# Optimization experiments

Hardware: AMD Instinct MI355X
Metric: run time of the kernel (lower is better)

The kernel has to match this reference:

```python
import jax, jax.numpy as jnp
import numpy as np

B, N, E, D, N_NODE = 512, 64, 64, 256, 200000
NEG = -9e15
ALPHA = 0.2  # leaky-relu slope from HGNN_ATT(..., 0.2, ...)


def _hgat_layer(x, adj_mask, w2, w3, a, a2, wc, w=None):
    """HyperGraphAttentionLayerSparse (HyperGAT), dense-masked vectorized form.
    x: [B,N,d_in], adj_mask: [B,E,N] bool. Returns (node [B,N,d], edge [B,E,d]).
    Eval mode: dropout is identity. concat=False so no ELU on output."""
    d = w2.shape[1]
    x4 = x @ w2                                            # [B,N,d]
    if w is not None:                                      # transfer=True path
        x = x @ w
    # node->edge attention: score = leakyrelu([word_context; x4_node] @ a), independent of edge idx
    s1 = jax.nn.leaky_relu(jnp.dot(wc, a[:d, 0]) + x4 @ a[d:, 0], ALPHA)   # [B,N]
    att_edge = jax.nn.softmax(jnp.where(adj_mask, s1[:, None, :], NEG), axis=2)  # [B,E,N]
    edge = att_edge @ x                                    # [B,E,d]
    edge4 = edge @ w3                                      # [B,E,d]
    # edge->node attention: score = leakyrelu([x4_node; edge4_edge] @ a2)
    s_pair = jax.nn.leaky_relu((x4 @ a2[:d, 0])[:, None, :] + (edge4 @ a2[d:, 0])[:, :, None], ALPHA)  # [B,E,N]
    att_node = jax.nn.softmax(jnp.swapaxes(jnp.where(adj_mask, s_pair, NEG), 1, 2), axis=2)  # [B,N,E]
    node = att_node @ edge                                 # [B,N,d]
    return node, edge


def setup_inputs() -> dict:
    key = jax.random.key(0)
    ks = jax.random.split(key, 16)
    stdv = 1.0 / np.sqrt(D)  # SessionGraph.reset_parameters uniform(-stdv, stdv)
    u = lambda k, shape: jax.random.uniform(k, shape, jnp.float32, -stdv, stdv)
    return {
        "inputs": jax.random.randint(ks[0], (B, N), 0, N_NODE, dtype=jnp.int32),
        "HT": (jax.random.uniform(ks[1], (B, E, N)) < 0.3).astype(jnp.int32),
        "G": jnp.zeros((1,), jnp.float32),
        "EG": jnp.zeros((1,), jnp.float32),
        "emb_w": u(ks[2], (N_NODE, D)),
        "emb2_w": u(ks[3], (N_NODE, D)),
        "g1_w2": u(ks[4], (D, D)),
        "g1_w3": u(ks[5], (D, D)),
        "g1_a": u(ks[6], (2 * D, 1)),
        "g1_a2": u(ks[7], (2 * D, 1)),
        "g1_wc": u(ks[8], (D,)),
        "g2_w": u(ks[9], (D, D)),
        "g2_w2": u(ks[10], (D, D)),
        "g2_w3": u(ks[11], (D, D)),
        "g2_a": u(ks[12], (2 * D, 1)),
        "g2_a2": u(ks[13], (2 * D, 1)),
        "g2_wc": u(ks[14], (D,)),
    }


def reference(inputs, HT, G, EG, emb_w, emb2_w, g1_w2, g1_w3, g1_a, g1_a2, g1_wc,
              g2_w, g2_w2, g2_w3, g2_a, g2_a2, g2_wc):
    adj_mask = HT > 0
    x = emb_w[inputs]                                      # [B,N,D] embedding gather
    residual = x
    # HGNN_ATT with step=2: gat1 (transfer=False) + residual, gat2 (transfer=True) + residual
    x, _ = _hgat_layer(x, adj_mask, g1_w2, g1_w3, g1_a, g1_a2, g1_wc)
    x = x + residual
    x, _ = _hgat_layer(x, adj_mask, g2_w2, g2_w3, g2_a, g2_a2, g2_wc, g2_w)
    x = x + residual
    nodes2 = emb2_w[inputs]                                # second embedding gather
    return (x, x, nodes2)  # (nodes, hidden, nodes2); hidden aliases nodes in the original
```

## Files before the change

kernel.cpp:

```cpp
#include <hip/hip_runtime.h>

#define BB 512
#define NN 64
#define EE 64
#define DD 256
#define BND (BB * NN * DD)
#define SA 68

typedef __attribute__((ext_vector_type(8))) short s8v;
typedef __attribute__((ext_vector_type(4))) float f4v;
typedef __attribute__((ext_vector_type(8))) unsigned short u16x8;

__device__ __forceinline__ unsigned short f2bf(float f) {
    unsigned int x = __float_as_uint(f);
    x = x + 0x7fffu + ((x >> 16) & 1u);
    return (unsigned short)(x >> 16);
}
__device__ __forceinline__ float bf2f(unsigned short u) {
    return __uint_as_float(((unsigned int)u) << 16);
}
__device__ __forceinline__ float lrelu(float v) { return v > 0.f ? v : 0.2f * v; }

#define WS_PREP  0
#define WS_P3B   8192
#define WS_WFRAG 12288

__global__ void prep_dots(const float* __restrict__ w2a, const float* __restrict__ w3a,
                          const float* __restrict__ aa, const float* __restrict__ a2a,
                          const float* __restrict__ wca,
                          const float* __restrict__ w2b, const float* __restrict__ w3b,
                          const float* __restrict__ ab, const float* __restrict__ a2b,
                          const float* __restrict__ wcb,
                          float* __restrict__ prep, float* __restrict__ p3b_ws) {
    const int t = threadIdx.x;
    const int blk = blockIdx.x;
    const int layer = blk >> 3;
    const int r0 = (blk & 7) * 32;
    __shared__ float vhi[256], v2lo[256], v2hi[256], red[256];
    const float* w2 = layer ? w2b : w2a;
    const float* w3 = layer ? w3b : w3a;
    const float* av = layer ? ab : aa;
    const float* a2 = layer ? a2b : a2a;
    vhi[t] = av[256 + t];
    v2lo[t] = a2[t];
    v2hi[t] = a2[256 + t];
    __syncthreads();
    const int row = r0 + (t >> 3), q = t & 7;
    const float* w2r = w2 + (size_t)row * DD + q * 32;
    const float* w3r = w3 + (size_t)row * DD + q * 32;
    float s1 = 0.f, s2 = 0.f, s3 = 0.f;
    #pragma unroll
    for (int c = 0; c < 8; c++) {
        float4 v = *(const float4*)&w2r[c * 4];
        float4 u = *(const float4*)&w3r[c * 4];
        float4 p1 = *(const float4*)&vhi[q * 32 + c * 4];
        float4 p2 = *(const float4*)&v2lo[q * 32 + c * 4];
        float4 p3 = *(const float4*)&v2hi[q * 32 + c * 4];
        s1 = fmaf(v.x, p1.x, fmaf(v.y, p1.y, fmaf(v.z, p1.z, fmaf(v.w, p1.w, s1))));
        s2 = fmaf(v.x, p2.x, fmaf(v.y, p2.y, fmaf(v.z, p2.z, fmaf(v.w, p2.w, s2))));
        s3 = fmaf(u.x, p3.x, fmaf(u.y, p3.y, fmaf(u.z, p3.z, fmaf(u.w, p3.w, s3))));
    }
    s1 += __shfl_xor(s1, 1); s1 += __shfl_xor(s1, 2); s1 += __shfl_xor(s1, 4);
    s2 += __shfl_xor(s2, 1); s2 += __shfl_xor(s2, 2); s2 += __shfl_xor(s2, 4);
    s3 += __shfl_xor(s3, 1); s3 += __shfl_xor(s3, 2); s3 += __shfl_xor(s3, 4);
    if (q == 0) {
        if (layer == 0) { prep[row] = s1; prep[256 + row] = s2; prep[512 + row] = s3; }
        else { prep[1024 + row] = s1; prep[1280 + row] = s2; p3b_ws[row] = s3; }
    }
    if ((blk & 7) == 0) {
        red[t] = layer ? (wcb[t] * ab[t]) : (wca[t] * aa[t]);
        __syncthreads();
        for (int o = 128; o > 0; o >>= 1) { if (t < o) red[t] += red[t + o]; __syncthreads(); }
        if (t == 0) prep[layer ? 1792 : 768] = red[0];
    }
}

__global__ void prep2_pack(const float* __restrict__ wtr, const float* __restrict__ p3b_ws,
                           float* __restrict__ prep, unsigned short* __restrict__ wfrag) {
    const int t = threadIdx.x, blk = blockIdx.x;
    __shared__ float p3[256];
    if (blk < 8) {
        p3[t] = p3b_ws[t];
        __syncthreads();
        const int row = blk * 32 + (t >> 3), q = t & 7;
        const float* wr = wtr + (size_t)row * DD + q * 32;
        float s = 0.f;
        #pragma unroll
        for (int c = 0; c < 8; c++) {
            float4 v = *(const float4*)&wr[c * 4];
            float4 p = *(const float4*)&p3[q * 32 + c * 4];
            s = fmaf(v.x, p.x, fmaf(v.y, p.y, fmaf(v.z, p.z, fmaf(v.w, p.w, s))));
        }
        s += __shfl_xor(s, 1); s += __shfl_xor(s, 2); s += __shfl_xor(s, 4);
        if (q == 0) prep[1536 + row] = s;
    } else {
        int gid = (blk - 8) * 256 + t;
        int l = gid & 63, frag = gid >> 6;
        int kc = frag >> 4, nt = frag & 15;
        int kb = kc * 32 + (l >> 4) * 8;
        int n = nt * 16 + (l & 15);
        u16x8 u;
        #pragma unroll
        for (int j = 0; j < 8; j++) u[j] = f2bf(wtr[(size_t)(kb + j) * DD + n]);
        *(u16x8*)(wfrag + (size_t)gid * 8) = u;
    }
}

__launch_bounds__(512, 4)
__global__ void mega(const int* __restrict__ inputs, const int* __restrict__ HT,
                     const float* __restrict__ emb_w, const float* __restrict__ emb2_w,
                     const float* __restrict__ prep, const unsigned short* __restrict__ wfrag,
                     float* __restrict__ out) {
    __shared__ unsigned short bufA[256 * SA];
    __shared__ unsigned short RA[64 * SA];
    __shared__ unsigned short RB[64 * SA];
    __shared__ unsigned short RC[64 * SA];
    __shared__ unsigned short RD[64 * SA];
    __shared__ unsigned short pvs[6 * 256];
    __shared__ unsigned short Debf[64];
    __shared__ float dvs[384];
    __shared__ float db2[192];
    __shared__ float u1f[64], invdef[64], invdnf[64];
    __shared__ unsigned long long mE[64], mN[64];
    __shared__ int idxs[64];

    const int b = blockIdx.x;
    const int t = threadIdx.x;
    const int lane = t & 63;
    const int w8 = t >> 6;
    const int l15 = lane & 15, lh = lane >> 4;

    if (t < 64) idxs[t] = inputs[b * 64 + t];
    for (int i = t; i < 1536; i += 512) {
        int off = i + (((i >> 8) >= 3) ? 256 : 0);
        pvs[i] = f2bf(prep[off]);
    }
    {
        const int rw = t >> 3, q8 = t & 7;
        const int idx = inputs[b * 64 + rw];
        const float* src = emb_w + (size_t)idx * DD + q8 * 32;
        #pragma unroll
        for (int c = 0; c < 8; c++) {
            float4 v = ((const float4*)src)[c];
            ushort4 u;
            u.x = f2bf(v.x); u.y = f2bf(v.y); u.z = f2bf(v.z); u.w = f2bf(v.w);
            *(ushort4*)&bufA[rw * 264 + q8 * 32 + c * 4] = u;
        }
    }
    float4 n2r[8];
    #pragma unroll
    for (int c = 0; c < 8; c++) {
        int i = t + 512 * c;
        int n = i >> 6, cc = i & 63;
        int idx = inputs[b * 64 + n];
        n2r[c] = ((const float4*)(emb2_w + (size_t)idx * DD))[cc];
    }
    #pragma unroll
    for (int i = 0; i < 8; i++) {
        int e = w8 * 8 + i;
        int hx = HT[((size_t)b * EE + e) * NN + lane];
        unsigned long long m = __ballot(hx > 0);
        if (lane == 0) mE[e] = m;
    }
    __syncthreads();

    if (w8 < 4) {
        const int wtile = w8 * 16;
        const int j = (l15 < 6) ? l15 : 5;
        f4v acc = {0.f, 0.f, 0.f, 0.f};
        #pragma unroll
        for (int kc = 0; kc < 8; kc++) {
            s8v a = *(const s8v*)&bufA[(wtile + l15) * 264 + kc * 32 + lh * 8];
            s8v bv = *(const s8v*)&pvs[j * 256 + kc * 32 + lh * 8];
            acc = __builtin_amdgcn_mfma_f32_16x16x32_bf16(a, bv, acc, 0, 0, 0);
        }
        if (l15 < 6) {
            #pragma unroll
            for (int rg = 0; rg < 4; rg++)
                dvs[l15 * 64 + wtile + lh * 4 + rg] = acc[rg];
        }
    } else if (w8 == 4) {
        unsigned long long acc = 0ull;
        for (int e = 0; e < 64; e++) acc |= ((mE[e] >> lane) & 1ull) << e;
        mN[lane] = acc;
    }
    __syncthreads();

    const int wr = (w8 & 3) * 16;
    const int wc = (w8 >> 2) * 32;
    const int row0 = wr + lh * 4;

    {
        float s1l = lrelu(prep[768] + dvs[lane]);
        float g1 = s1l;
        #pragma unroll
        for (int o = 32; o > 0; o >>= 1) g1 = fmaxf(g1, __shfl_xor(g1, o));
        float E1 = __expf(s1l - g1);
        #pragma unroll
        for (int i = 0; i < 8; i++) {
            int e = w8 * 8 + i;
            unsigned long long me = mE[e];
            float pe = (me == 0ull) ? 1.f : (((me >> lane) & 1ull) ? E1 : 0.f);
            unsigned short bf = f2bf(pe);
            RA[lane * SA + e] = bf;
            RC[e * SA + lane] = bf;
        }
    }
    __syncthreads();

    if (w8 < 4) {
        const int etile = w8 * 16;
        f4v acc = {0.f, 0.f, 0.f, 0.f};
        #pragma unroll
        for (int kc = 0; kc < 2; kc++) {
            u16x8 au;
            #pragma unroll
            for (int jj = 0; jj < 8; jj++) {
                float v = (l15 == 0) ? 1.f : ((l15 == 1) ? dvs[128 + kc * 32 + lh * 8 + jj] : 0.f);
                au[jj] = f2bf(v);
            }
            s8v bv = *(const s8v*)&RC[(etile + l15) * SA + kc * 32 + lh * 8];
            acc = __builtin_amdgcn_mfma_f32_16x16x32_bf16((s8v)au, bv, acc, 0, 0, 0);
        }
        if (lh == 0) {
            int e = etile + l15;
            float De = acc[0], We = acc[1];
            invdef[e] = 1.f / De;
            u1f[e] = We / De;
            Debf[e] = f2bf(De);
        }
    }
    __syncthreads();

    {
        float t2l = dvs[64 + lane];
        float gt2 = t2l;
        #pragma unroll
        for (int o = 32; o > 0; o >>= 1) gt2 = fmaxf(gt2, __shfl_xor(gt2, o));
        float um = u1f[lane];
        #pragma unroll
        for (int o = 32; o > 0; o >>= 1) um = fmaxf(um, __shfl_xor(um, o));
        float M1 = lrelu(gt2 + um);
        float ul = u1f[lane];
        float ide = invdef[lane];
        #pragma unroll
        for (int i = 0; i < 8; i++) {
            int n = w8 * 8 + i;
            unsigned long long mn = mN[n];
            float t2n = dvs[64 + n];
            float pr = (mn == 0ull) ? 1.f
                     : (((mn >> lane) & 1ull) ? __expf(lrelu(t2n + ul) - M1) : 0.f);
            RB[n * SA + lane] = f2bf(pr * ide);
        }
    }
    __syncthreads();

    if (w8 < 4) {
        const int ntile = w8 * 16;
        f4v acc = {0.f, 0.f, 0.f, 0.f};
        #pragma unroll
        for (int kc = 0; kc < 2; kc++) {
            u16x8 au;
            #pragma unroll
            for (int jj = 0; jj < 8; jj++) au[jj] = Debf[kc * 32 + lh * 8 + jj];
            s8v bv = *(const s8v*)&RB[(ntile + l15) * SA + kc * 32 + lh * 8];
            acc = __builtin_amdgcn_mfma_f32_16x16x32_bf16((s8v)au, bv, acc, 0, 0, 0);
        }
        if (lh == 0) invdnf[ntile + l15] = 1.f / acc[0];
    }
    __syncthreads();

    {
        f4v a0 = {0.f,0.f,0.f,0.f}, a1 = {0.f,0.f,0.f,0.f};
        #pragma unroll
        for (int kc = 0; kc < 2; kc++) {
            s8v a  = *(const s8v*)&RB[(wr + l15) * SA + kc * 32 + lh * 8];
            s8v b0 = *(const s8v*)&RA[(wc + l15) * SA + kc * 32 + lh * 8];
            s8v b1 = *(const s8v*)&RA[(wc + 16 + l15) * SA + kc * 32 + lh * 8];
            a0 = __builtin_amdgcn_mfma_f32_16x16x32_bf16(a, b0, a0, 0, 0, 0);
            a1 = __builtin_amdgcn_mfma_f32_16x16x32_bf16(a, b1, a1, 0, 0, 0);
        }
        int col0 = wc + l15, col1 = wc + 16 + l15;
        ushort4 u0, u1;
        #pragma unroll
        for (int rg = 0; rg < 4; rg++) {
            float idn = invdnf[row0 + rg];
            unsigned short b0s = f2bf(a0[rg] * idn + ((row0 + rg) == col0 ? 1.f : 0.f));
            unsigned short b1s = f2bf(a1[rg] * idn + ((row0 + rg) == col1 ? 1.f : 0.f));
            ((unsigned short*)&u0)[rg] = b0s;
            ((unsigned short*)&u1)[rg] = b1s;
            RC[(row0 + rg) * SA + col0] = b0s;
            RC[(row0 + rg) * SA + col1] = b1s;
        }
        *(ushort4*)&RD[col0 * SA + row0] = u0;
        *(ushort4*)&RD[col1 * SA + row0] = u1;
    }
    __syncthreads();

    if (w8 < 4) {
        const int ntile = w8 * 16;
        f4v acc = {0.f, 0.f, 0.f, 0.f};
        #pragma unroll
        for (int kc = 0; kc < 2; kc++) {
            u16x8 au;
            #pragma unroll
            for (int jj = 0; jj < 8; jj++) {
                float v = (l15 < 3) ? dvs[192 + l15 * 64 + kc * 32 + lh * 8 + jj] : 0.f;
                au[jj] = f2bf(v);
            }
            s8v bv = *(const s8v*)&RC[(ntile + l15) * SA + kc * 32 + lh * 8];
            acc = __builtin_amdgcn_mfma_f32_16x16x32_bf16((s8v)au, bv, acc, 0, 0, 0);
        }
        if (lh == 0) {
            int n = ntile + l15;
            db2[n] = acc[0]; db2[64 + n] = acc[1]; db2[128 + n] = acc[2];
        }
    }
    __syncthreads();

    {
        float s2l = lrelu(prep[1792] + db2[lane]);
        float g2 = s2l;
        #pragma unroll
        for (int o = 32; o > 0; o >>= 1) g2 = fmaxf(g2, __shfl_xor(g2, o));
        float E2 = __expf(s2l - g2);
        #pragma unroll
        for (int i = 0; i < 8; i++) {
            int e = w8 * 8 + i;
            unsigned long long me = mE[e];
            float pe = (me == 0ull) ? 1.f : (((me >> lane) & 1ull) ? E2 : 0.f);
            unsigned short bf = f2bf(pe);
            RA[lane * SA + e] = bf;
            RC[e * SA + lane] = bf;
        }
    }
    __syncthreads();

    if (w8 < 4) {
        const int etile = w8 * 16;
        f4v acc = {0.f, 0.f, 0.f, 0.f};
        #pragma unroll
        for (int kc = 0; kc < 2; kc++) {
            u16x8 au;
            #pragma unroll
            for (int jj = 0; jj < 8; jj++) {
                float v = (l15 == 0) ? 1.f : ((l15 == 1) ? db2[128 + kc * 32 + lh * 8 + jj] : 0.f);
                au[jj] = f2bf(v);
            }
            s8v bv = *(const s8v*)&RC[(etile + l15) * SA + kc * 32 + lh * 8];
            acc = __builtin_amdgcn_mfma_f32_16x16x32_bf16((s8v)au, bv, acc, 0, 0, 0);
        }
        if (lh == 0) {
            int e = etile + l15;
            float De = acc[0], We = acc[1];
            invdef[e] = 1.f / De;
            u1f[e] = We / De;
            Debf[e] = f2bf(De);
        }
    }
    __syncthreads();

    {
        float d1l = db2[64 + lane];
        float gd1 = d1l;
        #pragma unroll
        for (int o = 32; o > 0; o >>= 1) gd1 = fmaxf(gd1, __shfl_xor(gd1, o));
        float um = u1f[lane];
        #pragma unroll
        for (int o = 32; o > 0; o >>= 1) um = fmaxf(um, __shfl_xor(um, o));
        float M2 = lrelu(gd1 + um);
        float ul = u1f[lane];
        float ide = invdef[lane];
        #pragma unroll
        for (int i = 0; i < 8; i++) {
            int n = w8 * 8 + i;
            unsigned long long mn = mN[n];
            float d1n = db2[64 + n];
            float pr = (mn == 0ull) ? 1.f
                     : (((mn >> lane) & 1ull) ? __expf(lrelu(d1n + ul) - M2) : 0.f);
            RB[n * SA + lane] = f2bf(pr * ide);
        }
    }
    __syncthreads();

    if (w8 < 4) {
        const int ntile = w8 * 16;
        f4v acc = {0.f, 0.f, 0.f, 0.f};
        #pragma unroll
        for (int kc = 0; kc < 2; kc++) {
            u16x8 au;
            #pragma unroll
            for (int jj = 0; jj < 8; jj++) au[jj] = Debf[kc * 32 + lh * 8 + jj];
            s8v bv = *(const s8v*)&RB[(ntile + l15) * SA + kc * 32 + lh * 8];
            acc = __builtin_amdgcn_mfma_f32_16x16x32_bf16((s8v)au, bv, acc, 0, 0, 0);
        }
        if (lh == 0) invdnf[ntile + l15] = 1.f / acc[0];
    }
    __syncthreads();

    {
        f4v a0 = {0.f,0.f,0.f,0.f}, a1 = {0.f,0.f,0.f,0.f};
        #pragma unroll
        for (int kc = 0; kc < 2; kc++) {
            s8v a  = *(const s8v*)&RB[(wr + l15) * SA + kc * 32 + lh * 8];
            s8v b0 = *(const s8v*)&RA[(wc + l15) * SA + kc * 32 + lh * 8];
            s8v b1 = *(const s8v*)&RA[(wc + 16 + l15) * SA + kc * 32 + lh * 8];
            a0 = __builtin_amdgcn_mfma_f32_16x16x32_bf16(a, b0, a0, 0, 0, 0);
            a1 = __builtin_amdgcn_mfma_f32_16x16x32_bf16(a, b1, a1, 0, 0, 0);
        }
        __syncthreads();
        #pragma unroll
        for (int rg = 0; rg < 4; rg++) {
            float idn = invdnf[row0 + rg];
            RC[(row0 + rg) * SA + wc + l15] = f2bf(a0[rg] * idn);
            RC[(row0 + rg) * SA + wc + 16 + l15] = f2bf(a1[rg] * idn);
        }
    }
    __syncthreads();

    {
        f4v a0 = {0.f,0.f,0.f,0.f}, a1 = {0.f,0.f,0.f,0.f};
        #pragma unroll
        for (int kc = 0; kc < 2; kc++) {
            s8v a  = *(const s8v*)&RC[(wr + l15) * SA + kc * 32 + lh * 8];
            s8v b0 = *(const s8v*)&RD[(wc + l15) * SA + kc * 32 + lh * 8];
            s8v b1 = *(const s8v*)&RD[(wc + 16 + l15) * SA + kc * 32 + lh * 8];
            a0 = __builtin_amdgcn_mfma_f32_16x16x32_bf16(a, b0, a0, 0, 0, 0);
            a1 = __builtin_amdgcn_mfma_f32_16x16x32_bf16(a, b1, a1, 0, 0, 0);
        }
        __syncthreads();
        #pragma unroll
        for (int rg = 0; rg < 4; rg++) {
            RA[(row0 + rg) * SA + wc + l15] = f2bf(a0[rg]);
            RA[(row0 + rg) * SA + wc + 16 + l15] = f2bf(a1[rg]);
        }
    }
    #pragma unroll
    for (int c = 0; c < 8; c++) {
        int i = t + 512 * c;
        int n = i >> 6, cc = i & 63;
        ((float4*)(out + (size_t)2 * BND + (size_t)(b * 64 + n) * DD))[cc] = n2r[c];
    }
    __syncthreads();

    const int cb8 = (w8 >> 2) * 8;
    unsigned short rres[8][4];
    {
        f4v acc[8];
        #pragma unroll
        for (int nt = 0; nt < 8; nt++) acc[nt] = (f4v){0.f, 0.f, 0.f, 0.f};
        const s8v* wf = (const s8v*)wfrag;
        #pragma unroll
        for (int kc = 0; kc < 8; kc++) {
            s8v a = *(const s8v*)&bufA[(wr + l15) * 264 + kc * 32 + lh * 8];
            #pragma unroll
            for (int nt = 0; nt < 8; nt++) {
                s8v bv = wf[(size_t)(kc * 16 + cb8 + nt) * 64 + lane];
                acc[nt] = __builtin_amdgcn_mfma_f32_16x16x32_bf16(a, bv, acc[nt], 0, 0, 0);
            }
        }
        #pragma unroll
        for (int nt = 0; nt < 8; nt++) {
            #pragma unroll
            for (int rg = 0; rg < 4; rg++)
                rres[nt][rg] = bufA[(row0 + rg) * 264 + (cb8 + nt) * 16 + l15];
        }
        __syncthreads();
        #pragma unroll
        for (int nt = 0; nt < 8; nt++) {
            int feat = (cb8 + nt) * 16 + l15;
            ushort4 u;
            u.x = f2bf(acc[nt][0]); u.y = f2bf(acc[nt][1]);
            u.z = f2bf(acc[nt][2]); u.w = f2bf(acc[nt][3]);
            *(ushort4*)&bufA[feat * SA + row0] = u;
        }
    }
    __syncthreads();

    {
        f4v acc2[8];
        #pragma unroll
        for (int nt = 0; nt < 8; nt++) acc2[nt] = (f4v){0.f, 0.f, 0.f, 0.f};
        #pragma unroll
        for (int kc = 0; kc < 2; kc++) {
            s8v a = *(const s8v*)&RA[(wr + l15) * SA + kc * 32 + lh * 8];
            #pragma unroll
            for (int nt = 0; nt < 8; nt++) {
                s8v bv = *(const s8v*)&bufA[((cb8 + nt) * 16 + l15) * SA + kc * 32 + lh * 8];
                acc2[nt] = __builtin_amdgcn_mfma_f32_16x16x32_bf16(a, bv, acc2[nt], 0, 0, 0);
            }
        }
        #pragma unroll
        for (int nt = 0; nt < 8; nt++) {
            #pragma unroll
            for (int rg = 0; rg < 4; rg++) {
                int row = row0 + rg;
                int colg = (cb8 + nt) * 16 + l15;
                float v = acc2[nt][rg] + bf2f(rres[nt][rg]);
                size_t o = (size_t)(b * 64 + row) * DD + colg;
                out[o] = v;
                out[BND + o] = v;
            }
        }
    }
}

extern "C" void kernel_launch(void* const* d_in, const int* in_sizes, int n_in,
                              void* d_out, int out_size, void* d_ws, size_t ws_size,
                              hipStream_t stream) {
    const int* inputs = (const int*)d_in[0];
    const int* HT = (const int*)d_in[1];
    const float* emb_w  = (const float*)d_in[4];
    const float* emb2_w = (const float*)d_in[5];
    const float* g1_w2 = (const float*)d_in[6];
    const float* g1_w3 = (const float*)d_in[7];
    const float* g1_a  = (const float*)d_in[8];
    const float* g1_a2 = (const float*)d_in[9];
    const float* g1_wc = (const float*)d_in[10];
    const float* g2_w  = (const float*)d_in[11];
    const float* g2_w2 = (const float*)d_in[12];
    const float* g2_w3 = (const float*)d_in[13];
    const float* g2_a  = (const float*)d_in[14];
    const float* g2_a2 = (const float*)d_in[15];
    const float* g2_wc = (const float*)d_in[16];

    float* out = (float*)d_out;
    float* prep = (float*)((char*)d_ws + WS_PREP);
    float* p3b_ws = (float*)((char*)d_ws + WS_P3B);
    unsigned short* wfrag = (unsigned short*)((char*)d_ws + WS_WFRAG);

    prep_dots<<<16, 256, 0, stream>>>(g1_w2, g1_w3, g1_a, g1_a2, g1_wc,
                                      g2_w2, g2_w3, g2_a, g2_a2, g2_wc,
                                      prep, p3b_ws);
    prep2_pack<<<40, 256, 0, stream>>>(g2_w, p3b_ws, prep, wfrag);
    mega<<<BB, 512, 0, stream>>>(inputs, HT, emb_w, emb2_w, prep, wfrag, out);
}
```

Baseline: 64.61 us.

## Fold node-normalizer and projection MFMAs into main attention matmul, drop barriers

Computes the per-node softmax denominator and the projected dot-products as an extra MFMA column tile alongside the attention-times-edge matmul, using a small XT staging matrix, instead of separate MFMA passes each followed by a block barrier. The normalizer is broadcast with a shuffle rather than through shared memory, and db2 is derived algebraically from the combined tile. This removes several __syncthreads and LDS round trips per layer. It adds bf16 rounding on the folded projections and removes two barriers, which carries some race risk.

```diff
diff --git a/kernel.cpp b/kernel.cpp
--- a/kernel.cpp
+++ b/kernel.cpp
@@ -116,13 +116,12 @@
     __shared__ unsigned short RB[64 * SA];
     __shared__ unsigned short RC[64 * SA];
     __shared__ unsigned short RD[64 * SA];
+    __shared__ unsigned short XT[16 * SA];
     __shared__ unsigned short pvs[6 * 256];
-    __shared__ unsigned short Debf[64];
     __shared__ float dvs[384];
     __shared__ float db2[192];
-    __shared__ float u1f[64], invdef[64], invdnf[64];
+    __shared__ float u1f[64], invdef[64];
     __shared__ unsigned long long mE[64], mN[64];
-    __shared__ int idxs[64];
 
     const int b = blockIdx.x;
     const int t = threadIdx.x;
@@ -130,11 +129,11 @@
     const int w8 = t >> 6;
     const int l15 = lane & 15, lh = lane >> 4;
 
-    if (t < 64) idxs[t] = inputs[b * 64 + t];
     for (int i = t; i < 1536; i += 512) {
         int off = i + (((i >> 8) >= 3) ? 256 : 0);
         pvs[i] = f2bf(prep[off]);
     }
+    for (int i = t; i < 16 * SA; i += 512) XT[i] = 0;
     {
         const int rw = t >> 3, q8 = t & 7;
         const int idx = inputs[b * 64 + rw];
@@ -216,18 +215,23 @@
             u16x8 au;
             #pragma unroll
             for (int jj = 0; jj < 8; jj++) {
-                float v = (l15 == 0) ? 1.f : ((l15 == 1) ? dvs[128 + kc * 32 + lh * 8 + jj] : 0.f);
+                int k = kc * 32 + lh * 8 + jj;
+                float v = (l15 == 0) ? 1.f : ((l15 <= 4) ? dvs[(l15 + 1) * 64 + k] : 0.f);
                 au[jj] = f2bf(v);
             }
             s8v bv = *(const s8v*)&RC[(etile + l15) * SA + kc * 32 + lh * 8];
             acc = __builtin_amdgcn_mfma_f32_16x16x32_bf16((s8v)au, bv, acc, 0, 0, 0);
         }
+        int e = etile + l15;
         if (lh == 0) {
-            int e = etile + l15;
             float De = acc[0], We = acc[1];
             invdef[e] = 1.f / De;
             u1f[e] = We / De;
-            Debf[e] = f2bf(De);
+            XT[e] = f2bf(De);
+            XT[1 * SA + e] = f2bf(acc[2]);
+            XT[2 * SA + e] = f2bf(acc[3]);
+        } else if (lh == 1) {
+            XT[3 * SA + e] = f2bf(acc[0]);
         }
     }
     __syncthreads();
@@ -255,65 +259,35 @@
     }
     __syncthreads();
 
-    if (w8 < 4) {
-        const int ntile = w8 * 16;
-        f4v acc = {0.f, 0.f, 0.f, 0.f};
-        #pragma unroll
-        for (int kc = 0; kc < 2; kc++) {
-            u16x8 au;
-            #pragma unroll
-            for (int jj = 0; jj < 8; jj++) au[jj] = Debf[kc * 32 + lh * 8 + jj];
-            s8v bv = *(const s8v*)&RB[(ntile + l15) * SA + kc * 32 + lh * 8];
-            acc = __builtin_amdgcn_mfma_f32_16x16x32_bf16((s8v)au, bv, acc, 0, 0, 0);
-        }
-        if (lh == 0) invdnf[ntile + l15] = 1.f / acc[0];
-    }
-    __syncthreads();
-
-    {
-        f4v a0 = {0.f,0.f,0.f,0.f}, a1 = {0.f,0.f,0.f,0.f};
+    {
+        f4v a0 = {0.f,0.f,0.f,0.f}, a1 = {0.f,0.f,0.f,0.f}, ax = {0.f,0.f,0.f,0.f};
         #pragma unroll
         for (int kc = 0; kc < 2; kc++) {
             s8v a  = *(const s8v*)&RB[(wr + l15) * SA + kc * 32 + lh * 8];
             s8v b0 = *(const s8v*)&RA[(wc + l15) * SA + kc * 32 + lh * 8];
             s8v b1 = *(const s8v*)&RA[(wc + 16 + l15) * SA + kc * 32 + lh * 8];
+            s8v bx = *(const s8v*)&XT[l15 * SA + kc * 32 + lh * 8];
             a0 = __builtin_amdgcn_mfma_f32_16x16x32_bf16(a, b0, a0, 0, 0, 0);
             a1 = __builtin_amdgcn_mfma_f32_16x16x32_bf16(a, b1, a1, 0, 0, 0);
-        }
+            ax = __builtin_amdgcn_mfma_f32_16x16x32_bf16(a, bx, ax, 0, 0, 0);
+        }
+        float invdn[4];
+        #pragma unroll
+        for (int rg = 0; rg < 4; rg++) invdn[rg] = 1.f / __shfl(ax[rg], lh << 4);
         int col0 = wc + l15, col1 = wc + 16 + l15;
         ushort4 u0, u1;
         #pragma unroll
         for (int rg = 0; rg < 4; rg++) {
-            float idn = invdnf[row0 + rg];
-            unsigned short b0s = f2bf(a0[rg] * idn + ((row0 + rg) == col0 ? 1.f : 0.f));
-            unsigned short b1s = f2bf(a1[rg] * idn + ((row0 + rg) == col1 ? 1.f : 0.f));
-            ((unsigned short*)&u0)[rg] = b0s;
-            ((unsigned short*)&u1)[rg] = b1s;
-            RC[(row0 + rg) * SA + col0] = b0s;
-            RC[(row0 + rg) * SA + col1] = b1s;
+            ((unsigned short*)&u0)[rg] = f2bf(a0[rg] * invdn[rg] + ((row0 + rg) == col0 ? 1.f : 0.f));
+            ((unsigned short*)&u1)[rg] = f2bf(a1[rg] * invdn[rg] + ((row0 + rg) == col1 ? 1.f : 0.f));
         }
         *(ushort4*)&RD[col0 * SA + row0] = u0;
         *(ushort4*)&RD[col1 * SA + row0] = u1;
-    }
-    __syncthreads();
-
-    if (w8 < 4) {
-        const int ntile = w8 * 16;
-        f4v acc = {0.f, 0.f, 0.f, 0.f};
-        #pragma unroll
-        for (int kc = 0; kc < 2; kc++) {
-            u16x8 au;
-            #pragma unroll
-            for (int jj = 0; jj < 8; jj++) {
-                float v = (l15 < 3) ? dvs[192 + l15 * 64 + kc * 32 + lh * 8 + jj] : 0.f;
-                au[jj] = f2bf(v);
-            }
-            s8v bv = *(const s8v*)&RC[(ntile + l15) * SA + kc * 32 + lh * 8];
-            acc = __builtin_amdgcn_mfma_f32_16x16x32_bf16((s8v)au, bv, acc, 0, 0, 0);
-        }
-        if (lh == 0) {
-            int n = ntile + l15;
-            db2[n] = acc[0]; db2[64 + n] = acc[1]; db2[128 + n] = acc[2];
+        if (w8 < 4 && l15 >= 1 && l15 <= 3) {
+            int jj = l15 - 1;
+            #pragma unroll
+            for (int rg = 0; rg < 4; rg++)
+                db2[jj * 64 + row0 + rg] = ax[rg] * invdn[rg] + dvs[(jj + 3) * 64 + row0 + rg];
         }
     }
     __syncthreads();
@@ -344,7 +318,8 @@
             u16x8 au;
             #pragma unroll
             for (int jj = 0; jj < 8; jj++) {
-                float v = (l15 == 0) ? 1.f : ((l15 == 1) ? db2[128 + kc * 32 + lh * 8 + jj] : 0.f);
+                int k = kc * 32 + lh * 8 + jj;
+                float v = (l15 == 0) ? 1.f : ((l15 == 1) ? db2[128 + k] : 0.f);
                 au[jj] = f2bf(v);
             }
             s8v bv = *(const s8v*)&RC[(etile + l15) * SA + kc * 32 + lh * 8];
@@ -355,7 +330,7 @@
             float De = acc[0], We = acc[1];
             invdef[e] = 1.f / De;
             u1f[e] = We / De;
-            Debf[e] = f2bf(De);
+            XT[e] = f2bf(De);
         }
     }
     __syncthreads();
@@ -383,37 +358,25 @@
     }
     __syncthreads();
 
-    if (w8 < 4) {
-        const int ntile = w8 * 16;
-        f4v acc = {0.f, 0.f, 0.f, 0.f};
-        #pragma unroll
-        for (int kc = 0; kc < 2; kc++) {
-            u16x8 au;
-            #pragma unroll
-            for (int jj = 0; jj < 8; jj++) au[jj] = Debf[kc * 32 + lh * 8 + jj];
-            s8v bv = *(const s8v*)&RB[(ntile + l15) * SA + kc * 32 + lh * 8];
-            acc = __builtin_amdgcn_mfma_f32_16x16x32_bf16((s8v)au, bv, acc, 0, 0, 0);
-        }
-        if (lh == 0) invdnf[ntile + l15] = 1.f / acc[0];
-    }
-    __syncthreads();
-
-    {
-        f4v a0 = {0.f,0.f,0.f,0.f}, a1 = {0.f,0.f,0.f,0.f};
+    {
+        f4v a0 = {0.f,0.f,0.f,0.f}, a1 = {0.f,0.f,0.f,0.f}, ax = {0.f,0.f,0.f,0.f};
         #pragma unroll
         for (int kc = 0; kc < 2; kc++) {
             s8v a  = *(const s8v*)&RB[(wr + l15) * SA + kc * 32 + lh * 8];
             s8v b0 = *(const s8v*)&RA[(wc + l15) * SA + kc * 32 + lh * 8];
             s8v b1 = *(const s8v*)&RA[(wc + 16 + l15) * SA + kc * 32 + lh * 8];
+            s8v bx = *(const s8v*)&XT[l15 * SA + kc * 32 + lh * 8];
             a0 = __builtin_amdgcn_mfma_f32_16x16x32_bf16(a, b0, a0, 0, 0, 0);
             a1 = __builtin_amdgcn_mfma_f32_16x16x32_bf16(a, b1, a1, 0, 0, 0);
-        }
-        __syncthreads();
+            ax = __builtin_amdgcn_mfma_f32_16x16x32_bf16(a, bx, ax, 0, 0, 0);
+        }
+        float invdn[4];
+        #pragma unroll
+        for (int rg = 0; rg < 4; rg++) invdn[rg] = 1.f / __shfl(ax[rg], lh << 4);
         #pragma unroll
         for (int rg = 0; rg < 4; rg++) {
-            float idn = invdnf[row0 + rg];
-            RC[(row0 + rg) * SA + wc + l15] = f2bf(a0[rg] * idn);
-            RC[(row0 + rg) * SA + wc + 16 + l15] = f2bf(a1[rg] * idn);
+            RC[(row0 + rg) * SA + wc + l15] = f2bf(a0[rg] * invdn[rg]);
+            RC[(row0 + rg) * SA + wc + 16 + l15] = f2bf(a1[rg] * invdn[rg]);
         }
     }
     __syncthreads();
@@ -428,7 +391,6 @@
             a0 = __builtin_amdgcn_mfma_f32_16x16x32_bf16(a, b0, a0, 0, 0, 0);
             a1 = __builtin_amdgcn_mfma_f32_16x16x32_bf16(a, b1, a1, 0, 0, 0);
         }
-        __syncthreads();
         #pragma unroll
         for (int rg = 0; rg < 4; rg++) {
             RA[(row0 + rg) * SA + wc + l15] = f2bf(a0[rg]);
```

New measurement: 64.00 us (median of 2 runs). No clear change (-0.9%).
